# Performance work log

Hardware: AMD Instinct MI355X
Metric: run time of the kernel (lower is better)

Reference implementation:

```python
import jax, jax.numpy as jnp
import numpy as np

N_NODES = 100000
N_EDGES = 1600000
IN_FEAT = 512
HIDDEN = 128
N_CLASSES = 7


def gcn_conv(x, edge_index, edge_weight, W, b):
    """PyG GCNConv: add self-loops (weight 1), symmetric normalization, linear, scatter-add, bias."""
    n = x.shape[0]
    src = jnp.concatenate([edge_index[0], jnp.arange(n, dtype=edge_index.dtype)])
    dst = jnp.concatenate([edge_index[1], jnp.arange(n, dtype=edge_index.dtype)])
    w = jnp.concatenate([edge_weight, jnp.ones((n,), dtype=edge_weight.dtype)])
    deg = jax.ops.segment_sum(w, dst, num_segments=n)  # degree on destination (col)
    dinv = jnp.where(deg > 0, jax.lax.rsqrt(deg), 0.0)
    norm = dinv[src] * w * dinv[dst]                   # [E+N]
    h = x @ W                                          # [N, out] transform BEFORE propagate
    msg = h[src] * norm[:, None]                       # [E+N, out] irregular gather
    out = jax.ops.segment_sum(msg, dst, num_segments=n)  # scatter-reduce
    return out + b


def setup_inputs() -> dict:
    key = jax.random.key(0)
    k1, k2, k3, k4, k5, k6 = jax.random.split(key, 6)
    x = jax.random.normal(k1, (N_NODES, IN_FEAT), dtype=jnp.float32)
    edge_index = jax.random.randint(k2, (2, N_EDGES), 0, N_NODES, dtype=jnp.int32)
    edge_weight = jax.random.uniform(k3, (N_EDGES,), dtype=jnp.float32)
    s1 = 1.0 / np.sqrt(IN_FEAT)
    s2 = 1.0 / np.sqrt(HIDDEN)
    W1 = jax.random.uniform(k4, (IN_FEAT, HIDDEN), dtype=jnp.float32, minval=-s1, maxval=s1)
    b1 = jnp.zeros((HIDDEN,), dtype=jnp.float32)
    W2 = jax.random.uniform(k5, (HIDDEN, N_CLASSES), dtype=jnp.float32, minval=-s2, maxval=s2)
    b2 = jnp.zeros((N_CLASSES,), dtype=jnp.float32)
    return {"x": x, "edge_index": edge_index, "edge_weight": edge_weight,
            "W1": W1, "b1": b1, "W2": W2, "b2": b2}


def reference(x, edge_index, edge_weight, W1, b1, W2, b2):
    # eval mode: F.dropout(training=False) is identity
    h = jax.nn.elu(gcn_conv(x, edge_index, edge_weight, W1, b1))
    out = gcn_conv(h, edge_index, edge_weight, W2, b2)
    return jax.nn.log_softmax(out, axis=1)
```

## Files before the change

### kernel.cpp

```cpp
#include <hip/hip_runtime.h>
#include <math.h>

#define N_NODES 100000
#define N_EDGES 1600000
#define IN_F 512
#define HID 128
#define NCLS 7

#define DEG_SHIFT 43
#define DEG_WMASK ((1ull << 43) - 1)
#define DEG_SCALE 4194304.0f
#define DEG_INV_SCALE (1.0f / 4194304.0f)
#define NB_SCAN 98

typedef short short8 __attribute__((ext_vector_type(8)));
typedef float f32x4 __attribute__((ext_vector_type(4)));
typedef unsigned long long u64;

__device__ __forceinline__ unsigned pack_bf16x2(float a, float b) {
  unsigned ua = __float_as_uint(a), ub = __float_as_uint(b);
  unsigned ra = (ua + 0x7FFFu + ((ua >> 16) & 1u)) >> 16;
  unsigned rb = (ub + 0x7FFFu + ((ub >> 16) & 1u)) >> 16;
  return ra | (rb << 16);
}
__device__ __forceinline__ unsigned short f32_to_bf16(float v) {
  unsigned u = __float_as_uint(v);
  return (unsigned short)((u + 0x7FFFu + ((u >> 16) & 1u)) >> 16);
}
__device__ __forceinline__ float bf_lo(unsigned u) { return __uint_as_float(u << 16); }
__device__ __forceinline__ float bf_hi(unsigned u) { return __uint_as_float(u & 0xFFFF0000u); }

__global__ void k_deg(const int* __restrict__ ei, const float* __restrict__ ew,
                      unsigned long long* __restrict__ packed, int* __restrict__ rank) {
  int e = blockIdx.x * 256 + threadIdx.x;
  int d = ei[N_EDGES + e];
  u64 fx = (u64)(ew[e] * DEG_SCALE + 0.5f);
  u64 old = atomicAdd(&packed[d], (1ull << DEG_SHIFT) | fx);
  rank[e] = (int)(old >> DEG_SHIFT);
}

__global__ void k_mid(const unsigned long long* __restrict__ packed,
                      float* __restrict__ dinv, int* __restrict__ cnt, int* __restrict__ bsum,
                      const float* __restrict__ W1, uint4* __restrict__ w1bf,
                      uint2* __restrict__ csr_pad) {
  const int b = blockIdx.x, t = threadIdx.x;
  if (b >= NB_SCAN) {
    int idx = (b - NB_SCAN) * 256 + t;
    if (idx < 8) csr_pad[idx] = make_uint2(0u, 0u);
    int lane = idx & 63;
    int st = idx >> 6;
    int tt = st & 7, ss = st >> 3;
    int n = tt * 16 + (lane & 15);
    int k0 = ss * 32 + (lane >> 4) * 8;
    uint4 v;
    v.x = pack_bf16x2(W1[(size_t)(k0 + 0) * HID + n], W1[(size_t)(k0 + 1) * HID + n]);
    v.y = pack_bf16x2(W1[(size_t)(k0 + 2) * HID + n], W1[(size_t)(k0 + 3) * HID + n]);
    v.z = pack_bf16x2(W1[(size_t)(k0 + 4) * HID + n], W1[(size_t)(k0 + 5) * HID + n]);
    v.w = pack_bf16x2(W1[(size_t)(k0 + 6) * HID + n], W1[(size_t)(k0 + 7) * HID + n]);
    w1bf[idx] = v;
    return;
  }
  __shared__ int sh[256];
  int base = b * 1024;
  int v = 0;
#pragma unroll
  for (int q = 0; q < 4; q++) {
    int idx = base + t * 4 + q;
    if (idx < N_NODES) {
      unsigned long long p = packed[idx];
      int c = (int)(p >> DEG_SHIFT);
      cnt[idx] = c;
      dinv[idx] = rsqrtf((float)(p & DEG_WMASK) * DEG_INV_SCALE + 1.0f);
      v += c;
    }
  }
  sh[t] = v;
  __syncthreads();
  for (int o = 128; o > 0; o >>= 1) {
    if (t < o) sh[t] += sh[t + o];
    __syncthreads();
  }
  if (t == 0) bsum[b] = sh[0];
}

__global__ void k_scan_bsum(int* bsum, int nb) {
  if (threadIdx.x == 0 && blockIdx.x == 0) {
    int acc = 0;
    for (int i = 0; i < nb; i++) { int v = bsum[i]; bsum[i] = acc; acc += v; }
  }
}

__global__ void k_scan_final(const int* __restrict__ cnt, const int* __restrict__ bsum,
                             int* __restrict__ offs) {
  __shared__ int s[256];
  int t = threadIdx.x;
  int base = blockIdx.x * 1024;
  int v[4]; int sum = 0;
#pragma unroll
  for (int q = 0; q < 4; q++) {
    int idx = base + t * 4 + q;
    v[q] = (idx < N_NODES) ? cnt[idx] : 0;
    sum += v[q];
  }
  s[t] = sum;
  __syncthreads();
  for (int o = 1; o < 256; o <<= 1) {
    int x = (t >= o) ? s[t - o] : 0;
    __syncthreads();
    s[t] += x;
    __syncthreads();
  }
  int acc = s[t] - sum + bsum[blockIdx.x];
#pragma unroll
  for (int q = 0; q < 4; q++) {
    int idx = base + t * 4 + q;
    if (idx < N_NODES) offs[idx] = acc;
    acc += v[q];
  }
}

__global__ void k_fill(const int* __restrict__ ei, const float* __restrict__ ew,
                       const int* __restrict__ rank, const int* __restrict__ offs,
                       uint2* __restrict__ csr) {
  int e = blockIdx.x * 256 + threadIdx.x;
  int s = ei[e];
  int d = ei[N_EDGES + e];
  int p = offs[d] + rank[e];
  csr[p] = make_uint2((unsigned)s, __float_as_uint(ew[e]));
}

#define SLABSTRIDE 132
__global__ __launch_bounds__(256) void k_gemm1(const float* __restrict__ x,
                                               const uint4* __restrict__ w1bf,
                                               const float* __restrict__ dinv,
                                               unsigned short* __restrict__ h_u16) {
  __shared__ unsigned slab[4 * 16 * SLABSTRIDE];
  const int tid = threadIdx.x;
  const int lane = tid & 63;
  const int wv = tid >> 6;
  const int gw = blockIdx.x * 4 + wv;
  if (gw >= N_NODES / 16) return;
  const int m0 = gw * 16;
  unsigned* ws = slab + wv * 16 * SLABSTRIDE;
  const int l16 = lane & 15, quad = lane >> 4;

  f32x4 acc[8];
#pragma unroll
  for (int t = 0; t < 8; t++) acc[t] = (f32x4){0.f, 0.f, 0.f, 0.f};

#pragma unroll
  for (int hf = 0; hf < 2; hf++) {
#pragma unroll
    for (int b = 0; b < 2; b++) {
      float4 v[8];
#pragma unroll
      for (int i = 0; i < 8; i++) {
        int row = b * 8 + i;
        v[i] = *(const float4*)(x + (size_t)(m0 + row) * IN_F + hf * 256 + lane * 4);
      }
#pragma unroll
      for (int i = 0; i < 8; i++) {
        int row = b * 8 + i;
        unsigned lo = pack_bf16x2(v[i].x, v[i].y);
        unsigned hi = pack_bf16x2(v[i].z, v[i].w);
        *(uint2*)&ws[row * SLABSTRIDE + lane * 2] = make_uint2(lo, hi);
      }
    }
    __threadfence_block();
#pragma unroll
    for (int ks = 0; ks < 8; ks++) {
      short8 af = *(const short8*)&ws[l16 * SLABSTRIDE + ks * 16 + quad * 4];
      const uint4* bbase = w1bf + (size_t)(hf * 8 + ks) * 8 * 64 + lane;
#pragma unroll
      for (int t = 0; t < 8; t++) {
        uint4 bv = bbase[t * 64];
        acc[t] = __builtin_amdgcn_mfma_f32_16x16x32_bf16(af, *(const short8*)&bv,
                                                         acc[t], 0, 0, 0);
      }
    }
  }
  float df[4];
#pragma unroll
  for (int r = 0; r < 4; r++) df[r] = dinv[m0 + quad * 4 + r];
#pragma unroll
  for (int t = 0; t < 8; t++)
#pragma unroll
    for (int r = 0; r < 4; r++)
      h_u16[(size_t)(m0 + quad * 4 + r) * HID + t * 16 + l16] = f32_to_bf16(acc[t][r] * df[r]);
}

__global__ __launch_bounds__(256) void k_agg1(const unsigned* __restrict__ h_u,
    const float* __restrict__ dinv, const int* __restrict__ offs, const int* __restrict__ cnt,
    const uint2* __restrict__ csr, const float* __restrict__ b1,
    const float* __restrict__ W2, float* __restrict__ h2) {
  int i = blockIdx.x * 4 + (threadIdx.x >> 6);
  int lane = threadIdx.x & 63;
  if (i >= N_NODES) return;
  float w2a[NCLS], w2b[NCLS];
#pragma unroll
  for (int c = 0; c < NCLS; c++) {
    w2a[c] = W2[(size_t)(2 * lane) * NCLS + c];
    w2b[c] = W2[(size_t)(2 * lane + 1) * NCLS + c];
  }
  int start = offs[i], len = cnt[i];
  int end = start + len;
  float ax = 0.f, ay = 0.f;
  for (int p = start; p < end; p += 8) {
    uint2 e[8];
#pragma unroll
    for (int k = 0; k < 8; k++) e[k] = csr[p + k];
    unsigned u[8];
#pragma unroll
    for (int k = 0; k < 8; k++) u[k] = h_u[(size_t)e[k].x * 64 + lane];
#pragma unroll
    for (int k = 0; k < 8; k++) {
      float n = (k == 0 || p + k < end) ? __uint_as_float(e[k].y) : 0.f;
      ax = fmaf(bf_lo(u[k]), n, ax);
      ay = fmaf(bf_hi(u[k]), n, ay);
    }
  }
  float di = dinv[i];
  unsigned u = h_u[(size_t)i * 64 + lane];
  float2 bb = *(const float2*)(b1 + lane * 2);
  float vx = fmaf(di, ax + bf_lo(u), bb.x);
  float vy = fmaf(di, ay + bf_hi(u), bb.y);
  vx = vx > 0.f ? vx : expm1f(vx);
  vy = vy > 0.f ? vy : expm1f(vy);
  float s[NCLS];
#pragma unroll
  for (int c = 0; c < NCLS; c++) s[c] = fmaf(vy, w2b[c], vx * w2a[c]);
#pragma unroll
  for (int m = 1; m < 64; m <<= 1) {
#pragma unroll
    for (int c = 0; c < NCLS; c++) s[c] += __shfl_xor(s[c], m);
  }
  if (lane < 8) {
    float v = lane == 0 ? s[0] : lane == 1 ? s[1] : lane == 2 ? s[2] :
              lane == 3 ? s[3] : lane == 4 ? s[4] : lane == 5 ? s[5] : s[6];
    h2[(size_t)i * 8 + lane] = (lane < NCLS) ? v * di : 0.f;
  }
}

__global__ __launch_bounds__(256) void k_agg2(const float* __restrict__ h2,
    const float* __restrict__ dinv, const int* __restrict__ offs, const int* __restrict__ cnt,
    const uint2* __restrict__ csr, const float* __restrict__ b2, float* __restrict__ out) {
  int tid = threadIdx.x;
  int i = blockIdx.x * 32 + (tid >> 3);
  int f = tid & 7;
  if (i >= N_NODES) return;
  int start = offs[i], len = cnt[i];
  int end = start + len;
  float acc = 0.0f;
  for (int p = start; p < end; p += 4) {
    uint2 e0 = csr[p];
    uint2 e1 = csr[p + 1];
    uint2 e2 = csr[p + 2];
    uint2 e3 = csr[p + 3];
    float v0 = h2[(size_t)e0.x * 8 + f];
    float v1 = h2[(size_t)e1.x * 8 + f];
    float v2 = h2[(size_t)e2.x * 8 + f];
    float v3 = h2[(size_t)e3.x * 8 + f];
    float n0 = __uint_as_float(e0.y);
    float n1 = (p + 1 < end) ? __uint_as_float(e1.y) : 0.f;
    float n2 = (p + 2 < end) ? __uint_as_float(e2.y) : 0.f;
    float n3 = (p + 3 < end) ? __uint_as_float(e3.y) : 0.f;
    acc = fmaf(v0, n0, acc);
    acc = fmaf(v1, n1, acc);
    acc = fmaf(v2, n2, acc);
    acc = fmaf(v3, n3, acc);
  }
  float di = dinv[i];
  float v = fmaf(di, acc + h2[(size_t)i * 8 + f], (f < NCLS) ? b2[f] : 0.0f);
  float vm = (f < NCLS) ? v : -INFINITY;
#pragma unroll
  for (int o = 1; o < 8; o <<= 1) vm = fmaxf(vm, __shfl_xor(vm, o, 8));
  float ex = (f < NCLS) ? expf(v - vm) : 0.0f;
  float s8 = ex;
#pragma unroll
  for (int o = 1; o < 8; o <<= 1) s8 += __shfl_xor(s8, o, 8);
  float lse = logf(s8);
  if (f < NCLS) out[(size_t)i * NCLS + f] = v - vm - lse;
}

extern "C" void kernel_launch(void* const* d_in, const int* in_sizes, int n_in,
                              void* d_out, int out_size, void* d_ws, size_t ws_size,
                              hipStream_t stream) {
  const float* x  = (const float*)d_in[0];
  const int*   ei = (const int*)d_in[1];
  const float* ew = (const float*)d_in[2];
  const float* W1 = (const float*)d_in[3];
  const float* b1 = (const float*)d_in[4];
  const float* W2 = (const float*)d_in[5];
  const float* b2 = (const float*)d_in[6];
  float* out = (float*)d_out;

  char* w = (char*)d_ws;
  const size_t Npad  = ((size_t)N_NODES * 4 + 255) & ~(size_t)255;
  const size_t Npad8 = ((size_t)N_NODES * 8 + 255) & ~(size_t)255;
  const size_t Epad  = ((size_t)N_EDGES * 4 + 255) & ~(size_t)255;
  size_t off = 0;
  unsigned long long* packed = (unsigned long long*)(w + off); off += Npad8;
  float*    dinv     = (float*)(w + off);    off += Npad;
  int*      cnt      = (int*)(w + off);      off += Npad;
  int*      offs     = (int*)(w + off);      off += Npad;
  int*      bsum     = (int*)(w + off);      off += 1024;
  int*      rank     = (int*)(w + off);      off += Epad;
  uint2*    csr      = (uint2*)(w + off);    off += ((size_t)(N_EDGES + 8) * 8 + 255) & ~(size_t)255;
  uint4*    w1bf     = (uint4*)(w + off);    off += (size_t)8192 * 16;
  unsigned short* h_u16 = (unsigned short*)(w + off); off += (size_t)N_NODES * HID * 2;
  float*    h2       = (float*)(w + off);    off += (size_t)N_NODES * 8 * 4;

  hipMemsetAsync(packed, 0, Npad8, stream);

  k_deg<<<N_EDGES / 256, 256, 0, stream>>>(ei, ew, packed, rank);
  k_mid<<<NB_SCAN + 32, 256, 0, stream>>>(packed, dinv, cnt, bsum, W1, w1bf, csr + N_EDGES);
  k_scan_bsum<<<1, 64, 0, stream>>>(bsum, NB_SCAN);
  k_scan_final<<<NB_SCAN, 256, 0, stream>>>(cnt, bsum, offs);
  k_fill<<<N_EDGES / 256, 256, 0, stream>>>(ei, ew, rank, offs, csr);
  k_gemm1<<<(N_NODES / 16 + 3) / 4, 256, 0, stream>>>(x, w1bf, dinv, h_u16);
  k_agg1<<<(N_NODES + 3) / 4, 256, 0, stream>>>((const unsigned*)h_u16, dinv, offs, cnt,
                                                csr, b1, W2, h2);
  k_agg2<<<N_NODES / 32, 256, 0, stream>>>(h2, dinv, offs, cnt, csr, b2, out);
}
```

Measured before the change: 536.5 us.

## Merge CSR fill with first GEMM and fold block-sum scan into final scan

Fuses the CSR fill kernel and the first-layer GEMM into one launch. Every fifth block runs a GEMM tile and the other four scatter edges, so the latency-bound scatter can overlap the bandwidth-bound GEMM. Each final-scan block now sums the preceding block totals itself, which removes the single-thread block-sum scan kernel. The cost is that fill blocks also reserve the GEMM's large shared-memory slab, which may lower their occupancy, and there is a small amount of redundant per-block reduction work.

```diff
diff --git a/kernel.cpp b/kernel.cpp
--- a/kernel.cpp
+++ b/kernel.cpp
@@ -12,6 +12,9 @@
 #define DEG_SCALE 4194304.0f
 #define DEG_INV_SCALE (1.0f / 4194304.0f)
 #define NB_SCAN 98
+#define G_FILL 6250
+#define G_GEMM 1563
+#define G_MERGED (G_FILL + G_GEMM)
 
 typedef short short8 __attribute__((ext_vector_type(8)));
 typedef float f32x4 __attribute__((ext_vector_type(4)));
@@ -83,17 +86,19 @@
   if (t == 0) bsum[b] = sh[0];
 }
 
-__global__ void k_scan_bsum(int* bsum, int nb) {
-  if (threadIdx.x == 0 && blockIdx.x == 0) {
-    int acc = 0;
-    for (int i = 0; i < nb; i++) { int v = bsum[i]; bsum[i] = acc; acc += v; }
-  }
-}
-
 __global__ void k_scan_final(const int* __restrict__ cnt, const int* __restrict__ bsum,
                              int* __restrict__ offs) {
   __shared__ int s[256];
   int t = threadIdx.x;
+  int c = (t < NB_SCAN && t < blockIdx.x) ? bsum[t] : 0;
+  s[t] = c;
+  __syncthreads();
+  for (int o = 128; o > 0; o >>= 1) {
+    if (t < o) s[t] += s[t + o];
+    __syncthreads();
+  }
+  int block_off = s[0];
+  __syncthreads();
   int base = blockIdx.x * 1024;
   int v[4]; int sum = 0;
 #pragma unroll
@@ -110,7 +115,7 @@
     s[t] += x;
     __syncthreads();
   }
-  int acc = s[t] - sum + bsum[blockIdx.x];
+  int acc = s[t] - sum + block_off;
 #pragma unroll
   for (int q = 0; q < 4; q++) {
     int idx = base + t * 4 + q;
@@ -119,26 +124,30 @@
   }
 }
 
-__global__ void k_fill(const int* __restrict__ ei, const float* __restrict__ ew,
-                       const int* __restrict__ rank, const int* __restrict__ offs,
-                       uint2* __restrict__ csr) {
-  int e = blockIdx.x * 256 + threadIdx.x;
-  int s = ei[e];
-  int d = ei[N_EDGES + e];
-  int p = offs[d] + rank[e];
-  csr[p] = make_uint2((unsigned)s, __float_as_uint(ew[e]));
-}
-
 #define SLABSTRIDE 132
-__global__ __launch_bounds__(256) void k_gemm1(const float* __restrict__ x,
-                                               const uint4* __restrict__ w1bf,
-                                               const float* __restrict__ dinv,
-                                               unsigned short* __restrict__ h_u16) {
+__global__ __launch_bounds__(256) void k_fillgemm(
+    const int* __restrict__ ei, const float* __restrict__ ew,
+    const int* __restrict__ rank, const int* __restrict__ offs, uint2* __restrict__ csr,
+    const float* __restrict__ x, const uint4* __restrict__ w1bf,
+    const float* __restrict__ dinv, unsigned short* __restrict__ h_u16) {
   __shared__ unsigned slab[4 * 16 * SLABSTRIDE];
+  const int bx = blockIdx.x;
   const int tid = threadIdx.x;
+
+  if (bx % 5 != 0) {
+    int fb = bx - bx / 5 - 1;
+    int e = fb * 256 + tid;
+    int s = ei[e];
+    int d = ei[N_EDGES + e];
+    int p = offs[d] + rank[e];
+    csr[p] = make_uint2((unsigned)s, __float_as_uint(ew[e]));
+    return;
+  }
+
+  const int gb = bx / 5;
   const int lane = tid & 63;
   const int wv = tid >> 6;
-  const int gw = blockIdx.x * 4 + wv;
+  const int gw = gb * 4 + wv;
   if (gw >= N_NODES / 16) return;
   const int m0 = gw * 16;
   unsigned* ws = slab + wv * 16 * SLABSTRIDE;
@@ -314,10 +323,8 @@
 
   k_deg<<<N_EDGES / 256, 256, 0, stream>>>(ei, ew, packed, rank);
   k_mid<<<NB_SCAN + 32, 256, 0, stream>>>(packed, dinv, cnt, bsum, W1, w1bf, csr + N_EDGES);
-  k_scan_bsum<<<1, 64, 0, stream>>>(bsum, NB_SCAN);
   k_scan_final<<<NB_SCAN, 256, 0, stream>>>(cnt, bsum, offs);
-  k_fill<<<N_EDGES / 256, 256, 0, stream>>>(ei, ew, rank, offs, csr);
-  k_gemm1<<<(N_NODES / 16 + 3) / 4, 256, 0, stream>>>(x, w1bf, dinv, h_u16);
+  k_fillgemm<<<G_MERGED, 256, 0, stream>>>(ei, ew, rank, offs, csr, x, w1bf, dinv, h_u16);
   k_agg1<<<(N_NODES + 3) / 4, 256, 0, stream>>>((const unsigned*)h_u16, dinv, offs, cnt,
                                                 csr, b1, W2, h2);
   k_agg2<<<N_NODES / 32, 256, 0, stream>>>(h2, dinv, offs, cnt, csr, b2, out);
```

Measured after the change: 505.7 us. 5.7% less time.
